# Kernel tuning notes

Hardware: AMD Instinct MI355X
Metric: run time of the kernel (lower is better)

Reference implementation:

```python
import jax, jax.numpy as jnp
import numpy as np

B, S, E, H = 2, 2048, 1024, 16
D = E // H  # head dim = 64


def setup_inputs() -> dict:
    key = jax.random.key(0)
    ks = jax.random.split(key, 6)
    x = jax.random.normal(ks[0], (B, S, E), dtype=jnp.float32)
    attn_mask = jax.random.bernoulli(ks[1], 0.1, (B, S, S))  # True = masked
    scale = 1.0 / np.sqrt(E)
    w_kernel = jax.random.normal(ks[2], (E, 3 * E), dtype=jnp.float32) * scale
    w_bias = jax.random.normal(ks[3], (3 * E,), dtype=jnp.float32) * 0.02
    fc_kernel = jax.random.normal(ks[4], (E, E), dtype=jnp.float32) * scale
    fc_bias = jax.random.normal(ks[5], (E,), dtype=jnp.float32) * 0.02
    return {"x": x, "attn_mask": attn_mask, "w_kernel": w_kernel,
            "w_bias": w_bias, "fc_kernel": fc_kernel, "fc_bias": fc_bias}


def reference(x, attn_mask, w_kernel, w_bias, fc_kernel, fc_bias):
    b, s, e = x.shape
    qkv = jnp.einsum("bse,ef->bsf", x, w_kernel) + w_bias  # (B,S,3E)
    q, k, v = jnp.split(qkv, 3, axis=-1)

    def heads(t):  # (B,S,E) -> (B,H,S,D)
        return t.reshape(b, s, H, D).transpose(0, 2, 1, 3)

    q, k, v = heads(q), heads(k), heads(v)
    scores = jnp.einsum("bhqd,bhkd->bhqk", q, k) / jnp.sqrt(jnp.float32(D))
    # faithful quirk: masked positions are filled with 1e-9, not -inf
    scores = jnp.where(attn_mask[:, None, :, :], jnp.float32(1e-9), scores)
    A = jax.nn.softmax(scores, axis=-1)
    out = jnp.einsum("bhqk,bhkd->bhqd", A, v)  # (B,H,S,D)
    out = out.transpose(0, 2, 1, 3).reshape(b, s, e)
    # dropout is identity in eval mode
    return jnp.einsum("bse,ef->bsf", out, fc_kernel) + fc_bias
```

## Files before the change

### kernel.cpp

```cpp
#include <hip/hip_runtime.h>
#include <math.h>

#define BB 2
#define SS 2048
#define EE 1024
#define HH 16

typedef _Float16 f16;
typedef __attribute__((ext_vector_type(8))) _Float16 f16x8;
typedef __attribute__((ext_vector_type(4))) _Float16 f16x4;
typedef __attribute__((ext_vector_type(4))) float f32x4;

static __device__ __forceinline__ unsigned short hbits(float f) {
  f16 h = (f16)f;
  return __builtin_bit_cast(unsigned short, h);
}

__global__ __launch_bounds__(256) void cvt_f32_f16(
    const float* __restrict__ in, f16* __restrict__ out, int n)
{
  int i = (blockIdx.x * 256 + threadIdx.x) * 8;
  if (i >= n) return;
  float4 a = *(const float4*)(in + i);
  float4 b = *(const float4*)(in + i + 4);
  f16x8 o;
  o[0] = (f16)a.x; o[1] = (f16)a.y; o[2] = (f16)a.z; o[3] = (f16)a.w;
  o[4] = (f16)b.x; o[5] = (f16)b.y; o[6] = (f16)b.z; o[7] = (f16)b.w;
  *(f16x8*)(out + i) = o;
}

__global__ __launch_bounds__(256) void transpose_cvt(
    const float* __restrict__ in, f16* __restrict__ out, int K, int N)
{
  __shared__ float T[64][65];
  const int k0 = blockIdx.y * 64, n0 = blockIdx.x * 64;
  const int tr = threadIdx.x >> 4, tc = (threadIdx.x & 15) * 4;
#pragma unroll
  for (int i = 0; i < 4; ++i) {
    int r = tr + i * 16;
    *(float4*)&T[r][tc] = *(const float4*)(in + (size_t)(k0 + r) * N + n0 + tc);
  }
  __syncthreads();
#pragma unroll
  for (int i = 0; i < 4; ++i) {
    int nl = tr + i * 16;
    f16x4 v;
    v[0] = (f16)T[tc + 0][nl];
    v[1] = (f16)T[tc + 1][nl];
    v[2] = (f16)T[tc + 2][nl];
    v[3] = (f16)T[tc + 3][nl];
    *(f16x4*)(out + (size_t)(n0 + nl) * K + k0 + tc) = v;
  }
}

__global__ __launch_bounds__(256) void gemm_f16(
    const f16* __restrict__ A, const f16* __restrict__ Bt,
    const float* __restrict__ bias, int M, int N, int K, int mode,
    f16* __restrict__ oQK, f16* __restrict__ oVT, float* __restrict__ oF32)
{
  __shared__ f16 Ah[128][36];
  __shared__ f16 Bh[128][36];

  const int t = threadIdx.x;
  const int l = t & 63, w = t >> 6;
  const int l15 = l & 15, l4 = l >> 4;
  const int wr = w >> 1, wc = w & 1;
  const int n0 = blockIdx.x * 128, m0 = blockIdx.y * 128;

  const int srow = t >> 1, soff = (t & 1) * 16;
  const f16* Ap = A + (size_t)(m0 + srow) * K + soff;
  const f16* Bp = Bt + (size_t)(n0 + srow) * K + soff;

  f32x4 acc[4][4] = {};

  f16x8 ra0 = *(const f16x8*)(Ap);
  f16x8 ra1 = *(const f16x8*)(Ap + 8);
  f16x8 rb0 = *(const f16x8*)(Bp);
  f16x8 rb1 = *(const f16x8*)(Bp + 8);

  for (int k0 = 0; k0 < K; k0 += 32) {
    __syncthreads();
    *(f16x8*)&Ah[srow][soff]     = ra0;
    *(f16x8*)&Ah[srow][soff + 8] = ra1;
    *(f16x8*)&Bh[srow][soff]     = rb0;
    *(f16x8*)&Bh[srow][soff + 8] = rb1;
    __syncthreads();
    if (k0 + 32 < K) {
      ra0 = *(const f16x8*)(Ap + k0 + 32);
      ra1 = *(const f16x8*)(Ap + k0 + 40);
      rb0 = *(const f16x8*)(Bp + k0 + 32);
      rb1 = *(const f16x8*)(Bp + k0 + 40);
    }
    f16x8 af[4], bf[4];
#pragma unroll
    for (int mr = 0; mr < 4; ++mr)
      af[mr] = *(const f16x8*)&Ah[wr * 64 + mr * 16 + l15][l4 * 8];
#pragma unroll
    for (int nr = 0; nr < 4; ++nr)
      bf[nr] = *(const f16x8*)&Bh[wc * 64 + nr * 16 + l15][l4 * 8];
#pragma unroll
    for (int mr = 0; mr < 4; ++mr)
#pragma unroll
      for (int nr = 0; nr < 4; ++nr)
        acc[mr][nr] = __builtin_amdgcn_mfma_f32_16x16x32_f16(
            af[mr], bf[nr], acc[mr][nr], 0, 0, 0);
  }

  if (mode == 1) {
#pragma unroll
    for (int nr = 0; nr < 4; ++nr) {
      const int n = n0 + wc * 64 + nr * 16 + l15;
      const float bv = bias[n];
#pragma unroll
      for (int mr = 0; mr < 4; ++mr)
#pragma unroll
        for (int j = 0; j < 4; ++j) {
          const int m = m0 + wr * 64 + mr * 16 + l4 * 4 + j;
          oF32[(size_t)m * N + n] = acc[mr][nr][j] + bv;
        }
    }
  } else {
#pragma unroll
    for (int nr = 0; nr < 4; ++nr) {
      const int n = n0 + wc * 64 + nr * 16 + l15;
      const float bv = bias[n];
      if (n < 2048) {
#pragma unroll
        for (int mr = 0; mr < 4; ++mr)
#pragma unroll
          for (int j = 0; j < 4; ++j) {
            const int m = m0 + wr * 64 + mr * 16 + l4 * 4 + j;
            oQK[(size_t)m * 2048 + n] = (f16)(acc[mr][nr][j] + bv);
          }
      } else {
        const int hh = (n - 2048) >> 6;
        const int d = (n - 2048) & 63;
#pragma unroll
        for (int mr = 0; mr < 4; ++mr) {
          const int tok0 = m0 + wr * 64 + mr * 16 + l4 * 4;
          const int bq = tok0 >> 11, sq = tok0 & 2047;
          f16x4 v;
          v[0] = (f16)(acc[mr][nr][0] + bv);
          v[1] = (f16)(acc[mr][nr][1] + bv);
          v[2] = (f16)(acc[mr][nr][2] + bv);
          v[3] = (f16)(acc[mr][nr][3] + bv);
          *(f16x4*)(oVT + ((size_t)(bq * 16 + hh) * 64 + d) * SS + sq) = v;
        }
      }
    }
  }
}

__global__ __launch_bounds__(256) void attn_mfma(
    const f16* __restrict__ qkbuf, const f16* __restrict__ vT,
    const int* __restrict__ mask, f16* __restrict__ aout)
{
  __shared__ f16 Kt[32][72];
  __shared__ f16 Vt[64][40];
  __shared__ f16 Pl[4][16][40];
  __shared__ float Ll[4][16];

  const int t = threadIdx.x;
  const int w = t >> 6, l = t & 63, l15 = l & 15, l4 = l >> 4;
  const int bh = blockIdx.y, b = bh >> 4, h = bh & 15;
  const int q0 = blockIdx.x * 64 + w * 16;
  const int qtok = b * SS + q0 + l15;

  const f16x8 bq0 = *(const f16x8*)(qkbuf + (size_t)qtok * 2048 + h * 64 + l4 * 8);
  const f16x8 bq1 = *(const f16x8*)(qkbuf + (size_t)qtok * 2048 + h * 64 + 32 + l4 * 8);

  f32x4 acc[4] = {{0.f,0.f,0.f,0.f},{0.f,0.f,0.f,0.f},
                  {0.f,0.f,0.f,0.f},{0.f,0.f,0.f,0.f}};
  float lsum = 0.f;

  const int* mrow = mask + ((size_t)b * SS + q0 + l15) * SS;

  const int krow = t >> 3, kcb = (t & 7) * 8;
  const f16* ksrc = qkbuf + (size_t)(b * SS + krow) * 2048 + 1024 + h * 64 + kcb;
  const int vd = t >> 2, vkb = (t & 3) * 8;
  const f16* vsrc = vT + ((size_t)bh * 64 + vd) * SS + vkb;

  for (int kt = 0; kt < SS; kt += 32) {
    *(f16x8*)&Kt[krow][kcb] = *(const f16x8*)(ksrc + (size_t)kt * 2048);
    *(f16x8*)&Vt[vd][vkb]   = *(const f16x8*)(vsrc + kt);
    __syncthreads();

    float p[2][4];
#pragma unroll
    for (int g = 0; g < 2; ++g) {
      const int4 mv = *(const int4*)(mrow + kt + g * 16 + l4 * 4);
      const f16x8 a0 = *(const f16x8*)&Kt[g * 16 + l15][l4 * 8];
      const f16x8 a1 = *(const f16x8*)&Kt[g * 16 + l15][32 + l4 * 8];
      f32x4 S = __builtin_amdgcn_mfma_f32_16x16x32_f16(
          a0, bq0, (f32x4){0.f, 0.f, 0.f, 0.f}, 0, 0, 0);
      S = __builtin_amdgcn_mfma_f32_16x16x32_f16(a1, bq1, S, 0, 0, 0);
      p[g][0] = __expf(mv.x ? 1e-9f : S[0] * 0.125f);
      p[g][1] = __expf(mv.y ? 1e-9f : S[1] * 0.125f);
      p[g][2] = __expf(mv.z ? 1e-9f : S[2] * 0.125f);
      p[g][3] = __expf(mv.w ? 1e-9f : S[3] * 0.125f);
      unsigned int pk0 =
          (unsigned)hbits(p[g][0]) | ((unsigned)hbits(p[g][1]) << 16);
      unsigned int pk1 =
          (unsigned)hbits(p[g][2]) | ((unsigned)hbits(p[g][3]) << 16);
      unsigned int* dst = (unsigned int*)&Pl[w][l15][g * 16 + l4 * 4];
      dst[0] = pk0;
      dst[1] = pk1;
    }
    float ps = ((p[0][0] + p[0][1]) + (p[0][2] + p[0][3])) +
               ((p[1][0] + p[1][1]) + (p[1][2] + p[1][3]));
    ps += __shfl_xor(ps, 16);
    ps += __shfl_xor(ps, 32);
    lsum += ps;

    const f16x8 pa = *(const f16x8*)&Pl[w][l15][l4 * 8];
#pragma unroll
    for (int dg = 0; dg < 4; ++dg) {
      const f16x8 vb = *(const f16x8*)&Vt[dg * 16 + l15][l4 * 8];
      acc[dg] = __builtin_amdgcn_mfma_f32_16x16x32_f16(pa, vb, acc[dg], 0, 0, 0);
    }
    __syncthreads();
  }

  if (l4 == 0) Ll[w][l15] = lsum;
  __syncthreads();

#pragma unroll
  for (int r = 0; r < 4; ++r) {
    const float inv = 1.0f / Ll[w][l4 * 4 + r];
    const int tok = b * SS + q0 + l4 * 4 + r;
    f16* op = aout + (size_t)tok * EE + h * 64 + l15;
#pragma unroll
    for (int dg = 0; dg < 4; ++dg) op[dg * 16] = (f16)(acc[dg][r] * inv);
  }
}

extern "C" void kernel_launch(void* const* d_in, const int* in_sizes, int n_in,
                              void* d_out, int out_size, void* d_ws,
                              size_t ws_size, hipStream_t stream)
{
  (void)in_sizes; (void)n_in; (void)out_size; (void)ws_size;
  const float* x   = (const float*)d_in[0];
  const int* mask  = (const int*)d_in[1];
  const float* wk  = (const float*)d_in[2];
  const float* wb  = (const float*)d_in[3];
  const float* fck = (const float*)d_in[4];
  const float* fcb = (const float*)d_in[5];
  float* out       = (float*)d_out;

  char* ws = (char*)d_ws;
  size_t off = 0;
  f16* xh    = (f16*)(ws + off); off += (size_t)4096 * 1024 * 2;
  f16* Wt    = (f16*)(ws + off); off += (size_t)3072 * 1024 * 2;
  f16* fckT  = (f16*)(ws + off); off += (size_t)1024 * 1024 * 2;
  f16* qk    = (f16*)(ws + off); off += (size_t)4096 * 2048 * 2;
  f16* vT    = (f16*)(ws + off); off += (size_t)BB * HH * 64 * SS * 2;
  f16* aoutH = (f16*)(ws + off); off += (size_t)4096 * 1024 * 2;

  cvt_f32_f16<<<4096 * 1024 / (8 * 256), 256, 0, stream>>>(x, xh, 4096 * 1024);
  transpose_cvt<<<dim3(3072 / 64, 1024 / 64), 256, 0, stream>>>(wk, Wt, 1024, 3072);
  transpose_cvt<<<dim3(1024 / 64, 1024 / 64), 256, 0, stream>>>(fck, fckT, 1024, 1024);

  gemm_f16<<<dim3(3072 / 128, 4096 / 128), 256, 0, stream>>>(
      xh, Wt, wb, 4096, 3072, 1024, 0, qk, vT, nullptr);

  attn_mfma<<<dim3(SS / 64, BB * HH), 256, 0, stream>>>(qk, vT, mask, aoutH);

  gemm_f16<<<dim3(1024 / 128, 4096 / 128), 256, 0, stream>>>(
      aoutH, fckT, fcb, 4096, 1024, 1024, 1, nullptr, nullptr, out);
}
```

Before: 291.6 us.

## Bit-pack attention mask and restructure attention kernel with double-buffered swizzled tiles

```diff
diff --git a/kernel.cpp b/kernel.cpp
--- a/kernel.cpp
+++ b/kernel.cpp
@@ -10,11 +10,6 @@
 typedef __attribute__((ext_vector_type(8))) _Float16 f16x8;
 typedef __attribute__((ext_vector_type(4))) _Float16 f16x4;
 typedef __attribute__((ext_vector_type(4))) float f32x4;
-
-static __device__ __forceinline__ unsigned short hbits(float f) {
-  f16 h = (f16)f;
-  return __builtin_bit_cast(unsigned short, h);
-}
 
 __global__ __launch_bounds__(256) void cvt_f32_f16(
     const float* __restrict__ in, f16* __restrict__ out, int n)
@@ -51,6 +46,14 @@
     v[3] = (f16)T[tc + 3][nl];
     *(f16x4*)(out + (size_t)(n0 + nl) * K + k0 + tc) = v;
   }
+}
+
+__global__ __launch_bounds__(256) void pack_mask(
+    const int* __restrict__ m, unsigned long long* __restrict__ bits)
+{
+  const int i = blockIdx.x * 256 + threadIdx.x;
+  const unsigned long long bal = __ballot(m[i] != 0);
+  if ((threadIdx.x & 63) == 0) bits[i >> 6] = bal;
 }
 
 __global__ __launch_bounds__(256) void gemm_f16(
@@ -151,86 +154,125 @@
   }
 }
 
-__global__ __launch_bounds__(256) void attn_mfma(
+__global__ __launch_bounds__(256, 2) void attn_mfma(
     const f16* __restrict__ qkbuf, const f16* __restrict__ vT,
-    const int* __restrict__ mask, f16* __restrict__ aout)
-{
-  __shared__ f16 Kt[32][72];
-  __shared__ f16 Vt[64][40];
-  __shared__ f16 Pl[4][16][40];
-  __shared__ float Ll[4][16];
+    const unsigned long long* __restrict__ mbits, f16* __restrict__ aout)
+{
+  __shared__ f16 Kds[2][64 * 64];
+  __shared__ f16 Vds[2][64 * 64];
 
   const int t = threadIdx.x;
   const int w = t >> 6, l = t & 63, l15 = l & 15, l4 = l >> 4;
   const int bh = blockIdx.y, b = bh >> 4, h = bh & 15;
-  const int q0 = blockIdx.x * 64 + w * 16;
-  const int qtok = b * SS + q0 + l15;
-
-  const f16x8 bq0 = *(const f16x8*)(qkbuf + (size_t)qtok * 2048 + h * 64 + l4 * 8);
-  const f16x8 bq1 = *(const f16x8*)(qkbuf + (size_t)qtok * 2048 + h * 64 + 32 + l4 * 8);
-
-  f32x4 acc[4] = {{0.f,0.f,0.f,0.f},{0.f,0.f,0.f,0.f},
-                  {0.f,0.f,0.f,0.f},{0.f,0.f,0.f,0.f}};
-  float lsum = 0.f;
-
-  const int* mrow = mask + ((size_t)b * SS + q0 + l15) * SS;
-
-  const int krow = t >> 3, kcb = (t & 7) * 8;
-  const f16* ksrc = qkbuf + (size_t)(b * SS + krow) * 2048 + 1024 + h * 64 + kcb;
-  const int vd = t >> 2, vkb = (t & 3) * 8;
-  const f16* vsrc = vT + ((size_t)bh * 64 + vd) * SS + vkb;
-
-  for (int kt = 0; kt < SS; kt += 32) {
-    *(f16x8*)&Kt[krow][kcb] = *(const f16x8*)(ksrc + (size_t)kt * 2048);
-    *(f16x8*)&Vt[vd][vkb]   = *(const f16x8*)(vsrc + kt);
+  const int qbase = blockIdx.x * 128 + w * 32;
+
+  f16x8 q00, q01, q10, q11;
+  {
+    const size_t r0 = (size_t)(b * SS + qbase + l15) * 2048 + h * 64;
+    const size_t r1 = (size_t)(b * SS + qbase + 16 + l15) * 2048 + h * 64;
+    q00 = *(const f16x8*)(qkbuf + r0 + l4 * 8);
+    q01 = *(const f16x8*)(qkbuf + r0 + 32 + l4 * 8);
+    q10 = *(const f16x8*)(qkbuf + r1 + l4 * 8);
+    q11 = *(const f16x8*)(qkbuf + r1 + 32 + l4 * 8);
+  }
+
+  f32x4 accA[4] = {}, accB[4] = {};
+  float lsA = 0.f, lsB = 0.f;
+
+  const unsigned long long* mA = mbits + (size_t)(b * SS + qbase + l15) * 32;
+  const unsigned long long* mB = mbits + (size_t)(b * SS + qbase + 16 + l15) * 32;
+
+  const int srow = t >> 3;
+  const int scb  = (t & 7) * 8;
+  const int sws  = (srow & 7) << 3;
+  const f16* kb = qkbuf + (size_t)b * SS * 2048 + 1024 + h * 64 + scb;
+  const f16* vb = vT + ((size_t)bh * 64 + srow) * SS + scb;
+
+  f16x8 kr0, kr1, vr0, vr1;
+#define LOADT(kt)                                                         \
+  {                                                                       \
+    kr0 = *(const f16x8*)(kb + (size_t)((kt) + srow) * 2048);             \
+    kr1 = *(const f16x8*)(kb + (size_t)((kt) + srow + 32) * 2048);        \
+    vr0 = *(const f16x8*)(vb + (kt));                                     \
+    vr1 = *(const f16x8*)(vb + 32 * SS + (kt));                           \
+  }
+#define COMMIT(bi)                                                        \
+  {                                                                       \
+    *(f16x8*)&Kds[bi][srow * 64 + (scb ^ sws)]        = kr0;              \
+    *(f16x8*)&Kds[bi][(srow + 32) * 64 + (scb ^ sws)] = kr1;              \
+    *(f16x8*)&Vds[bi][srow * 64 + (scb ^ sws)]        = vr0;              \
+    *(f16x8*)&Vds[bi][(srow + 32) * 64 + (scb ^ sws)] = vr1;              \
+  }
+
+  LOADT(0)
+  COMMIT(0)
+  LOADT(64)
+  __syncthreads();
+
+  const int swr = (l15 & 7) << 3;
+
+  for (int tI = 0; tI < 32; ++tI) {
+    const int cur = tI & 1;
+    const unsigned long long mbA = mA[tI];
+    const unsigned long long mbB = mB[tI];
+
+#pragma unroll
+    for (int g = 0; g < 4; ++g) {
+      const f16* krow = &Kds[cur][(g * 16 + l15) * 64];
+      const f16x8 k0 = *(const f16x8*)(krow + ((l4 * 8) ^ swr));
+      const f16x8 k1 = *(const f16x8*)(krow + ((32 + l4 * 8) ^ swr));
+      f32x4 SA = __builtin_amdgcn_mfma_f32_16x16x32_f16(
+          k0, q00, (f32x4){0.f, 0.f, 0.f, 0.f}, 0, 0, 0);
+      SA = __builtin_amdgcn_mfma_f32_16x16x32_f16(k1, q01, SA, 0, 0, 0);
+      f32x4 SB = __builtin_amdgcn_mfma_f32_16x16x32_f16(
+          k0, q10, (f32x4){0.f, 0.f, 0.f, 0.f}, 0, 0, 0);
+      SB = __builtin_amdgcn_mfma_f32_16x16x32_f16(k1, q11, SB, 0, 0, 0);
+
+      const unsigned int nibA = (unsigned int)(mbA >> (g * 16 + l4 * 4));
+      const unsigned int nibB = (unsigned int)(mbB >> (g * 16 + l4 * 4));
+      f16x4 paA, paB;
+#pragma unroll
+      for (int j = 0; j < 4; ++j) {
+        const float pA = ((nibA >> j) & 1u) ? 1.0f : __expf(SA[j] * 0.125f);
+        const float pB = ((nibB >> j) & 1u) ? 1.0f : __expf(SB[j] * 0.125f);
+        lsA += pA;
+        lsB += pB;
+        paA[j] = (f16)pA;
+        paB[j] = (f16)pB;
+      }
+#pragma unroll
+      for (int dg = 0; dg < 4; ++dg) {
+        const f16x4 vf = *(const f16x4*)&Vds[cur][(dg * 16 + l15) * 64 +
+                                                  ((g * 16 + l4 * 4) ^ swr)];
+        accA[dg] = __builtin_amdgcn_mfma_f32_16x16x16f16(paA, vf, accA[dg], 0, 0, 0);
+        accB[dg] = __builtin_amdgcn_mfma_f32_16x16x16f16(paB, vf, accB[dg], 0, 0, 0);
+      }
+    }
+
+    if (tI + 1 < 32) {
+      COMMIT(cur ^ 1)
+      if (tI + 2 < 32) LOADT((tI + 2) * 64)
+    }
     __syncthreads();
-
-    float p[2][4];
-#pragma unroll
-    for (int g = 0; g < 2; ++g) {
-      const int4 mv = *(const int4*)(mrow + kt + g * 16 + l4 * 4);
-      const f16x8 a0 = *(const f16x8*)&Kt[g * 16 + l15][l4 * 8];
-      const f16x8 a1 = *(const f16x8*)&Kt[g * 16 + l15][32 + l4 * 8];
-      f32x4 S = __builtin_amdgcn_mfma_f32_16x16x32_f16(
-          a0, bq0, (f32x4){0.f, 0.f, 0.f, 0.f}, 0, 0, 0);
-      S = __builtin_amdgcn_mfma_f32_16x16x32_f16(a1, bq1, S, 0, 0, 0);
-      p[g][0] = __expf(mv.x ? 1e-9f : S[0] * 0.125f);
-      p[g][1] = __expf(mv.y ? 1e-9f : S[1] * 0.125f);
-      p[g][2] = __expf(mv.z ? 1e-9f : S[2] * 0.125f);
-      p[g][3] = __expf(mv.w ? 1e-9f : S[3] * 0.125f);
-      unsigned int pk0 =
-          (unsigned)hbits(p[g][0]) | ((unsigned)hbits(p[g][1]) << 16);
-      unsigned int pk1 =
-          (unsigned)hbits(p[g][2]) | ((unsigned)hbits(p[g][3]) << 16);
-      unsigned int* dst = (unsigned int*)&Pl[w][l15][g * 16 + l4 * 4];
-      dst[0] = pk0;
-      dst[1] = pk1;
-    }
-    float ps = ((p[0][0] + p[0][1]) + (p[0][2] + p[0][3])) +
-               ((p[1][0] + p[1][1]) + (p[1][2] + p[1][3]));
-    ps += __shfl_xor(ps, 16);
-    ps += __shfl_xor(ps, 32);
-    lsum += ps;
-
-    const f16x8 pa = *(const f16x8*)&Pl[w][l15][l4 * 8];
+  }
+
+  lsA += __shfl_xor(lsA, 16);
+  lsA += __shfl_xor(lsA, 32);
+  lsB += __shfl_xor(lsB, 16);
+  lsB += __shfl_xor(lsB, 32);
+
+#pragma unroll
+  for (int j = 0; j < 4; ++j) {
+    const int qr = l4 * 4 + j;
+    const float invA = 1.0f / __shfl(lsA, qr);
+    const float invB = 1.0f / __shfl(lsB, qr);
+    const size_t rowA = (size_t)(b * SS + qbase + qr) * EE + h * 64 + l15;
+    const size_t rowB = (size_t)(b * SS + qbase + 16 + qr) * EE + h * 64 + l15;
 #pragma unroll
     for (int dg = 0; dg < 4; ++dg) {
-      const f16x8 vb = *(const f16x8*)&Vt[dg * 16 + l15][l4 * 8];
-      acc[dg] = __builtin_amdgcn_mfma_f32_16x16x32_f16(pa, vb, acc[dg], 0, 0, 0);
-    }
-    __syncthreads();
-  }
-
-  if (l4 == 0) Ll[w][l15] = lsum;
-  __syncthreads();
-
-#pragma unroll
-  for (int r = 0; r < 4; ++r) {
-    const float inv = 1.0f / Ll[w][l4 * 4 + r];
-    const int tok = b * SS + q0 + l4 * 4 + r;
-    f16* op = aout + (size_t)tok * EE + h * 64 + l15;
-#pragma unroll
-    for (int dg = 0; dg < 4; ++dg) op[dg * 16] = (f16)(acc[dg][r] * inv);
+      aout[rowA + dg * 16] = (f16)(accA[dg][j] * invA);
+      aout[rowB + dg * 16] = (f16)(accB[dg][j] * invB);
+    }
   }
 }
 
@@ -255,15 +297,18 @@
   f16* qk    = (f16*)(ws + off); off += (size_t)4096 * 2048 * 2;
   f16* vT    = (f16*)(ws + off); off += (size_t)BB * HH * 64 * SS * 2;
   f16* aoutH = (f16*)(ws + off); off += (size_t)4096 * 1024 * 2;
+  unsigned long long* mbits = (unsigned long long*)(ws + off);
+  off += (size_t)BB * SS * SS / 8;
 
   cvt_f32_f16<<<4096 * 1024 / (8 * 256), 256, 0, stream>>>(x, xh, 4096 * 1024);
   transpose_cvt<<<dim3(3072 / 64, 1024 / 64), 256, 0, stream>>>(wk, Wt, 1024, 3072);
   transpose_cvt<<<dim3(1024 / 64, 1024 / 64), 256, 0, stream>>>(fck, fckT, 1024, 1024);
+  pack_mask<<<BB * SS * SS / 256, 256, 0, stream>>>(mask, mbits);
 
   gemm_f16<<<dim3(3072 / 128, 4096 / 128), 256, 0, stream>>>(
       xh, Wt, wb, 4096, 3072, 1024, 0, qk, vT, nullptr);
 
-  attn_mfma<<<dim3(SS / 64, BB * HH), 256, 0, stream>>>(qk, vT, mask, aoutH);
+  attn_mfma<<<dim3(SS / 128, BB * HH), 256, 0, stream>>>(qk, vT, mbits, aoutH);
 
   gemm_f16<<<dim3(1024 / 128, 4096 / 128), 256, 0, stream>>>(
       aoutH, fckT, fcb, 4096, 1024, 1024, 1, nullptr, nullptr, out);
```

After: 243.6 us. -16.5%, faster.
